# Kernel optimization log

Hardware: AMD Instinct MI355X
Metric: run time of the kernel (lower is better)

Reference implementation:

```python
import jax, jax.numpy as jnp
import numpy as np

K_MASK = -2.3819763e+38

B, T, D = 2, 2048, 2048
N_HEADS, N_KV, HEAD_DIM = 16, 8, 128
SCALAR = 0.08838834764831845  # head_dim ** -0.5
ROPE_BASE = 10000


def rms_norm(x, scale):
    # fp32 mean-of-squares, rsqrt, bf16 round-trip, then scale (as in QwemmaRMSNorm)
    x32 = x.astype(jnp.float32)
    var = jnp.mean(jnp.square(x32), axis=-1, keepdims=True)
    rescaled = (x32 * jax.lax.rsqrt(var + 1e-06)).astype(jnp.bfloat16)
    return rescaled * scale


def apply_rope(inputs, positions, base_frequency):
    head_dim = inputs.shape[-1]
    fraction = 2 * jnp.arange(0, head_dim // 2) / head_dim
    timescale = base_frequency ** fraction
    sinusoid = positions[..., jnp.newaxis] / timescale[jnp.newaxis, jnp.newaxis, :]
    sinusoid = sinusoid[..., jnp.newaxis, :]  # [B,T,1,H/2]
    sin = jnp.sin(sinusoid).astype(inputs.dtype)
    cos = jnp.cos(sinusoid).astype(inputs.dtype)
    first, second = jnp.split(inputs, 2, axis=-1)
    out = jnp.concatenate([first * cos - second * sin,
                           second * cos + first * sin], axis=-1)
    return out.astype(inputs.dtype)


def setup_inputs() -> dict:
    key = jax.random.key(0)
    ks = jax.random.split(key, 7)
    x = jax.random.normal(ks[0], (B, T, D), dtype=jnp.float32)
    segment_pos = jnp.broadcast_to(jnp.arange(T, dtype=jnp.int32)[None, :], (B, T))
    attn_mask = jnp.broadcast_to(jnp.tril(jnp.ones((T, T), dtype=bool))[None], (B, T, T))
    q_w = jax.random.normal(ks[1], (N_HEADS, D, HEAD_DIM), dtype=jnp.float32) * 0.02
    kv_w = jax.random.normal(ks[2], (2, N_KV, D, HEAD_DIM), dtype=jnp.float32) * 0.02
    o_w = jax.random.normal(ks[3], (N_HEADS, HEAD_DIM, D), dtype=jnp.float32) * 0.02
    q_scale = 1.0 + 0.1 * jax.random.normal(ks[4], (HEAD_DIM,), dtype=jnp.float32)
    k_scale = 1.0 + 0.1 * jax.random.normal(ks[5], (HEAD_DIM,), dtype=jnp.float32)
    return {"x": x, "segment_pos": segment_pos, "attn_mask": attn_mask,
            "q_w": q_w, "kv_w": kv_w, "o_w": o_w,
            "q_scale": q_scale, "k_scale": k_scale}


def reference(x, segment_pos, attn_mask, q_w, kv_w, o_w, q_scale, k_scale):
    # projections
    q = jnp.einsum('BTD,NDH->BTNH', x, q_w)
    k, v = jnp.einsum('BSD,CKDH->CBSKH', x, kv_w)
    # QK RMSNorm + RoPE
    q = apply_rope(rms_norm(q, q_scale), segment_pos, ROPE_BASE)
    k = apply_rope(rms_norm(k, k_scale), segment_pos, ROPE_BASE)
    # GQA: [B,T,N,H] -> [B,T,K,G,H]
    b, t, n, h = q.shape
    g = n // N_KV
    q = q.reshape((b, t, N_KV, g, h))
    logits = jnp.einsum('BTKGH,BSKH->BTKGS', q, k)
    logits = (logits.astype(jnp.float32) * SCALAR).astype(jnp.bfloat16)
    s = logits.shape[-1]
    logits = logits.reshape((b, t, n, s))
    padded = jnp.where(jnp.expand_dims(attn_mask, -2), logits, K_MASK)
    probs = jax.nn.softmax(padded.astype(jnp.float32), axis=-1).astype(k.dtype)
    probs = probs.reshape((b, t, N_KV, g, s))
    encoded = jnp.einsum('BTKGS,BSKH->BTKGH', probs, v)
    encoded = encoded.reshape((b, t, n, h))
    return jnp.einsum('BTNH,NHD->BTD', encoded, o_w)


if __name__ == '__main__':
    out = reference(**setup_inputs())
    print(out.shape, out.dtype)
```

## Files before the change

### kernel.cpp

```cpp
#include <hip/hip_runtime.h>

typedef unsigned short u16;
typedef __attribute__((ext_vector_type(4))) float f32x4;
typedef __attribute__((ext_vector_type(8))) short s16x8;

#define SCALAR_F 0.08838834764831845f
#define KMASKF (-1e30f)

__device__ __forceinline__ u16 f2b(float f){
  unsigned u = __float_as_uint(f);
  unsigned r = u + 0x7FFFu + ((u>>16)&1u);
  return (u16)(r>>16);
}
__device__ __forceinline__ float b2f(u16 h){ return __uint_as_float(((unsigned)h)<<16); }

__device__ __forceinline__ f32x4 mfma16(s16x8 a, s16x8 b, f32x4 c){
  return __builtin_amdgcn_mfma_f32_16x16x32_bf16(a, b, c, 0, 0, 0);
}

__device__ __forceinline__ void glds16(const u16* g, u16* l){
  __builtin_amdgcn_global_load_lds((const __attribute__((address_space(1))) unsigned*)g,
                                   (__attribute__((address_space(3))) unsigned*)l, 16, 0, 0);
}

__global__ __launch_bounds__(256) void cvt_f32_bf16(const float* __restrict__ in, u16* __restrict__ out){
  int i = blockIdx.x*256 + threadIdx.x;
  const float4* p = (const float4*)in;
  float4 a = p[2*i], b = p[2*i+1];
  s16x8 r;
  r[0]=(short)f2b(a.x); r[1]=(short)f2b(a.y); r[2]=(short)f2b(a.z); r[3]=(short)f2b(a.w);
  r[4]=(short)f2b(b.x); r[5]=(short)f2b(b.y); r[6]=(short)f2b(b.z); r[7]=(short)f2b(b.w);
  *(s16x8*)(out + (size_t)i*8) = r;
}

__global__ __launch_bounds__(256) void build_wqkvt(const float* __restrict__ qw, const float* __restrict__ kvw,
                                                   u16* __restrict__ out){
  __shared__ float t[64][65];
  int head = blockIdx.z;
  int d0 = blockIdx.y*64, h0 = blockIdx.x*64;
  const float* src; int colbase;
  if (head < 16){ src = qw + (size_t)head*2048*128; colbase = head*128; }
  else if (head < 24){ int k = head-16; src = kvw + (size_t)k*2048*128; colbase = 2048 + k*128; }
  else { int k = head-24; src = kvw + (size_t)(8+k)*2048*128; colbase = 3072 + k*128; }
  int tid = threadIdx.x;
  #pragma unroll
  for (int p=0;p<16;p++){ int e = p*256+tid; int r = e>>6, c = e&63;
    t[r][c] = src[(size_t)(d0+r)*128 + h0 + c]; }
  __syncthreads();
  #pragma unroll
  for (int p=0;p<16;p++){ int e = p*256+tid; int c = e>>6, r = e&63;
    out[(size_t)(colbase + h0 + c)*2048 + d0 + r] = f2b(t[r][c]); }
}

__global__ __launch_bounds__(256) void tr2048(const float* __restrict__ src, u16* __restrict__ out){
  __shared__ float t[64][65];
  int r0 = blockIdx.y*64, c0 = blockIdx.x*64;
  int tid = threadIdx.x;
  #pragma unroll
  for (int p=0;p<16;p++){ int e = p*256+tid; int r = e>>6, c = e&63;
    t[r][c] = src[(size_t)(r0+r)*2048 + c0 + c]; }
  __syncthreads();
  #pragma unroll
  for (int p=0;p<16;p++){ int e = p*256+tid; int c = e>>6, r = e&63;
    out[(size_t)(c0+c)*2048 + r0 + r] = f2b(t[r][c]); }
}

__global__ __launch_bounds__(256) void rope_table(float* __restrict__ table){
  int tid = blockIdx.x*256 + threadIdx.x;
  int pos = tid>>6, i = tid&63;
  float ts = powf(10000.f, (float)i * (1.f/64.f));
  float ang = (float)pos / ts;
  ((float2*)table)[tid] = make_float2(sinf(ang), cosf(ang));
}

template<bool OUTBF16>
__global__ __launch_bounds__(256) void gemm_bt(const u16* __restrict__ A, const u16* __restrict__ Bt,
                                               void* __restrict__ C, int K, int ldc){
  __shared__ u16 As[128*64];
  __shared__ u16 Bs[128*64];
  const int tid = threadIdx.x, w = tid>>6, l = tid&63;
  const int wm = w>>1, wn = w&1;
  const int l15 = l&15, lg = l>>4, l7 = l&7;
  const size_t m0 = (size_t)blockIdx.y*128, n0 = (size_t)blockIdx.x*128;
  const f32x4 z4 = {0.f,0.f,0.f,0.f};
  f32x4 acc[4][4];
  #pragma unroll
  for (int m=0;m<4;m++)
    #pragma unroll
    for (int n=0;n<4;n++) acc[m][n] = z4;
  const char* AsB = (const char*)As; const char* BsB = (const char*)Bs;
  int colsw[2];
  colsw[0] = (lg*16) ^ (l7<<4);
  colsw[1] = (64 + lg*16) ^ (l7<<4);
  int arow[4], brow[4];
  #pragma unroll
  for (int m=0;m<4;m++){ arow[m] = (wm*64 + m*16 + l15)*128; brow[m] = (wn*64 + m*16 + l15)*128; }
  const int sgl = l7 ^ (l>>3);
  for (int k0=0;k0<K;k0+=64){
    #pragma unroll
    for (int i=0;i<4;i++){
      int slot = (w*4+i)*64 + l;
      int row = slot>>3;
      glds16(A  + (m0+row)*K + k0 + sgl*8, (u16*)As + slot*8);
      glds16(Bt + (n0+row)*K + k0 + sgl*8, (u16*)Bs + slot*8);
    }
    __syncthreads();
    #pragma unroll
    for (int kb=0;kb<2;kb++){
      s16x8 af[4], bf[4];
      #pragma unroll
      for (int m=0;m<4;m++) af[m] = *(const s16x8*)(AsB + arow[m] + colsw[kb]);
      #pragma unroll
      for (int n=0;n<4;n++) bf[n] = *(const s16x8*)(BsB + brow[n] + colsw[kb]);
      #pragma unroll
      for (int m=0;m<4;m++)
        #pragma unroll
        for (int n=0;n<4;n++)
          acc[m][n] = mfma16(af[m], bf[n], acc[m][n]);
    }
    __syncthreads();
  }
  #pragma unroll
  for (int m=0;m<4;m++)
    #pragma unroll
    for (int n=0;n<4;n++)
      #pragma unroll
      for (int r=0;r<4;r++){
        size_t row = m0 + wm*64 + m*16 + lg*4 + r;
        size_t col = n0 + wn*64 + n*16 + l15;
        if (OUTBF16) ((u16*)C)[row*ldc + col] = f2b(acc[m][n][r]);
        else ((float*)C)[row*ldc + col] = acc[m][n][r];
      }
}

__global__ __launch_bounds__(256) void norm_rope(const u16* __restrict__ qkv, const float* __restrict__ table,
                                                 const float* __restrict__ scale, const int* __restrict__ segpos,
                                                 u16* __restrict__ dst, int nhl2, int colbase, float mult){
  int w = threadIdx.x>>6, l = threadIdx.x&63;
  int rid = blockIdx.x*4 + w;
  int bt = rid >> nhl2;
  int n  = rid & ((1<<nhl2)-1);
  int b = bt >> 11, t = bt & 2047;
  const u16* src = qkv + (size_t)bt*4096 + colbase + n*128;
  float x1 = b2f(src[l]), x2 = b2f(src[64+l]);
  float ss = x1*x1 + x2*x2;
  #pragma unroll
  for (int off=32; off; off>>=1) ss += __shfl_xor(ss, off);
  float rs = rsqrtf(ss*(1.f/128.f) + 1e-6f);
  float v1 = x1*rs*scale[l], v2 = x2*rs*scale[64+l];
  int pos = segpos[bt];
  float2 sc = ((const float2*)table)[pos*64 + l];
  float o1 = (v1*sc.y - v2*sc.x)*mult;
  float o2 = (v2*sc.y + v1*sc.x)*mult;
  u16* d = dst + (((size_t)((b<<nhl2) + n))*2048 + t)*128;
  d[l] = f2b(o1); d[64+l] = f2b(o2);
}

__global__ __launch_bounds__(256) void vtr(const u16* __restrict__ qkv, u16* __restrict__ vt){
  __shared__ float t[64][65];
  int bk = blockIdx.z;
  int t0 = blockIdx.y*64, d0 = blockIdx.x*64;
  int b = bk>>3, kv = bk&7;
  int tid = threadIdx.x;
  #pragma unroll
  for (int p=0;p<16;p++){ int e = p*256+tid; int r = e>>6, c = e&63;
    t[r][c] = b2f(qkv[(size_t)(b*2048 + t0 + r)*4096 + 3072 + kv*128 + d0 + c]); }
  __syncthreads();
  #pragma unroll
  for (int p=0;p<16;p++){ int e = p*256+tid; int c = e>>6, r = e&63;
    vt[((size_t)bk*128 + d0 + c)*2048 + t0 + r] = f2b(t[r][c]); }
}

__global__ __launch_bounds__(256,4) void attn_kern(const u16* __restrict__ qn, const u16* __restrict__ kn,
                                                   const u16* __restrict__ vt, u16* __restrict__ enc){
  __shared__ u16 Ks[64*128];
  __shared__ u16 Vs[128*64];
  __shared__ u16 Ps[4*16*64];
  const int idx = blockIdx.x;
  const int qb = 31 - (idx>>5);
  const int hb = idx & 31;
  const int hn = hb & 15, b = hb >> 4;
  const int t0 = qb*64;
  const int kv = hn>>1;
  const int tid = threadIdx.x, w = tid>>6, l = tid&63;
  const int l15 = l&15, lg = l>>4;
  const u16* qh = qn + ((size_t)(b*16+hn))*2048*128;
  const u16* kh = kn + ((size_t)(b*8+kv))*2048*128;
  const u16* vh = vt + ((size_t)(b*8+kv))*128*2048;
  const int qr0 = t0 + w*16;

  s16x8 qf[4];
  #pragma unroll
  for (int kb=0;kb<4;kb++)
    qf[kb] = *(const s16x8*)(qh + (size_t)(qr0 + l15)*128 + kb*32 + lg*8);

  const f32x4 z4 = {0.f,0.f,0.f,0.f};
  f32x4 o[8];
  #pragma unroll
  for (int dn=0;dn<8;dn++) o[dn] = z4;
  float mrow[4], lp[4];
  #pragma unroll
  for (int r=0;r<4;r++){ mrow[r] = KMASKF; lp[r] = 0.f; }

  const char* KsB = (const char*)Ks;
  const char* VsB = (const char*)Vs;
  char* PsB = (char*)Ps + w*2048;

  const int ntiles = qb + 1;
  for (int it=0; it<ntiles; ++it){
    int s0 = it*64;
    #pragma unroll
    for (int i=0;i<4;i++){
      int slot = (w*4+i)*64 + l;
      { int row = slot>>4, g = slot&15, gl = g ^ (row&7);
        glds16(kh + (size_t)(s0+row)*128 + gl*8, Ks + slot*8); }
      { int row = slot>>3, g = slot&7, gl = g ^ (row&7);
        glds16(vh + (size_t)row*2048 + s0 + gl*8, Vs + slot*8); }
    }
    __syncthreads();

    f32x4 sa[4];
    #pragma unroll
    for (int nc=0;nc<4;nc++) sa[nc] = z4;
    #pragma unroll
    for (int kb=0;kb<4;kb++){
      s16x8 kf[4];
      #pragma unroll
      for (int nc=0;nc<4;nc++){
        int srow = nc*16 + l15;
        int cb = (kb*64 + lg*16) ^ ((srow&7)<<4);
        kf[nc] = *(const s16x8*)(KsB + srow*256 + cb);
      }
      #pragma unroll
      for (int nc=0;nc<4;nc++)
        sa[nc] = mfma16(qf[kb], kf[nc], sa[nc]);
    }
    if (it == ntiles-1){
      #pragma unroll
      for (int nc=0;nc<4;nc++)
        #pragma unroll
        for (int r=0;r<4;r++){
          int row = qr0 + lg*4 + r;
          int col = s0 + nc*16 + l15;
          if (col > row) sa[nc][r] = KMASKF;
        }
    }
    #pragma unroll
    for (int r=0;r<4;r++){
      float pm = fmaxf(fmaxf(sa[0][r], sa[1][r]), fmaxf(sa[2][r], sa[3][r]));
      pm = fmaxf(pm, __shfl_xor(pm,1));
      pm = fmaxf(pm, __shfl_xor(pm,2));
      pm = fmaxf(pm, __shfl_xor(pm,4));
      pm = fmaxf(pm, __shfl_xor(pm,8));
      float mo = mrow[r];
      float mn = fmaxf(mo, pm);
      float sc = __expf(mo - mn);
      mrow[r] = mn;
      int rowp = lg*4 + r;
      float ls = 0.f;
      #pragma unroll
      for (int nc=0;nc<4;nc++){
        float p = __expf(sa[nc][r] - mn);
        ls += p;
        int cb = ((nc*16 + l15)*2) ^ ((rowp&7)<<4);
        *(u16*)(PsB + rowp*128 + cb) = f2b(p);
      }
      lp[r] = lp[r]*sc + ls;
      #pragma unroll
      for (int dn=0;dn<8;dn++) o[dn][r] *= sc;
    }
    asm volatile("" ::: "memory");
    #pragma unroll
    for (int kb=0;kb<2;kb++){
      int rowp = l15;
      int cbp = (kb*64 + lg*16) ^ ((rowp&7)<<4);
      s16x8 pf = *(const s16x8*)(PsB + rowp*128 + cbp);
      #pragma unroll
      for (int dn=0;dn<8;dn++){
        int vrow = dn*16 + l15;
        int cb = (kb*64 + lg*16) ^ ((vrow&7)<<4);
        s16x8 vf = *(const s16x8*)(VsB + vrow*128 + cb);
        o[dn] = mfma16(pf, vf, o[dn]);
      }
    }
    __syncthreads();
  }
  #pragma unroll
  for (int r=0;r<4;r++){
    float s = lp[r];
    s += __shfl_xor(s,1); s += __shfl_xor(s,2); s += __shfl_xor(s,4); s += __shfl_xor(s,8);
    lp[r] = 1.f/s;
  }
  #pragma unroll
  for (int dn=0;dn<8;dn++)
    #pragma unroll
    for (int r=0;r<4;r++){
      size_t row = (size_t)b*2048 + qr0 + lg*4 + r;
      size_t col = hn*128 + dn*16 + l15;
      enc[row*2048 + col] = f2b(o[dn][r]*lp[r]);
    }
}

extern "C" void kernel_launch(void* const* d_in, const int* in_sizes, int n_in,
                              void* d_out, int out_size, void* d_ws, size_t ws_size,
                              hipStream_t stream){
  const float* x      = (const float*)d_in[0];
  const int*   segpos = (const int*)d_in[1];
  const float* qw     = (const float*)d_in[3];
  const float* kvw    = (const float*)d_in[4];
  const float* ow     = (const float*)d_in[5];
  const float* qs     = (const float*)d_in[6];
  const float* ks     = (const float*)d_in[7];
  float* out = (float*)d_out;

  char* ws = (char*)d_ws;
  size_t off = 0;
  auto alloc = [&](size_t bytes)->void*{ void* p = ws + off; off += (bytes + 255) & ~(size_t)255; return p; };
  u16*   xb    = (u16*)alloc((size_t)4096*2048*2);
  u16*   wqkvt = (u16*)alloc((size_t)4096*2048*2);
  u16*   wot   = (u16*)alloc((size_t)2048*2048*2);
  u16*   qkv   = (u16*)alloc((size_t)4096*4096*2);
  u16*   qn    = (u16*)alloc((size_t)2*16*2048*128*2);
  u16*   kn    = (u16*)alloc((size_t)2*8*2048*128*2);
  u16*   vt    = (u16*)alloc((size_t)2*8*128*2048*2);
  u16*   enc   = (u16*)alloc((size_t)4096*2048*2);
  float* table = (float*)alloc((size_t)2048*64*2*4);

  cvt_f32_bf16<<<4096,256,0,stream>>>(x, xb);
  build_wqkvt<<<dim3(2,32,32),256,0,stream>>>(qw, kvw, wqkvt);
  tr2048<<<dim3(32,32),256,0,stream>>>(ow, wot);
  rope_table<<<512,256,0,stream>>>(table);
  gemm_bt<true><<<dim3(32,32),256,0,stream>>>(xb, wqkvt, qkv, 2048, 4096);
  norm_rope<<<16384,256,0,stream>>>(qkv, table, qs, segpos, qn, 4, 0,    SCALAR_F);
  norm_rope<<<8192, 256,0,stream>>>(qkv, table, ks, segpos, kn, 3, 2048, 1.0f);
  vtr<<<dim3(2,32,16),256,0,stream>>>(qkv, vt);
  attn_kern<<<1024,256,0,stream>>>(qn, kn, vt, enc);
  gemm_bt<false><<<dim3(16,32),256,0,stream>>>(enc, wot, out, 2048, 2048);
}
```

Measured before the change: 438.0 us.

## Pair causal query blocks per workgroup and double-buffer K/V tiles in LDS

Each attention workgroup now handles two query blocks, pp and 31-pp, so every workgroup runs exactly 33 KV tiles and the causal triangle's work is balanced. K/V tiles are double-buffered in LDS, and the next tile's global-to-LDS loads are issued before computing on the current one, overlapping memory with MFMA work. The grid is halved to 512 workgroups and launch bounds drop to 2 blocks per CU. The larger LDS footprint and fewer workgroups may reduce occupancy.

Result: faster. 384.7 us (-12.2%).

```diff
diff --git a/kernel.cpp b/kernel.cpp
--- a/kernel.cpp
+++ b/kernel.cpp
@@ -171,24 +171,24 @@
     vt[((size_t)bk*128 + d0 + c)*2048 + t0 + r] = f2b(t[r][c]); }
 }
 
-__global__ __launch_bounds__(256,4) void attn_kern(const u16* __restrict__ qn, const u16* __restrict__ kn,
+__global__ __launch_bounds__(256,2) void attn_kern(const u16* __restrict__ qn, const u16* __restrict__ kn,
                                                    const u16* __restrict__ vt, u16* __restrict__ enc){
-  __shared__ u16 Ks[64*128];
-  __shared__ u16 Vs[128*64];
+  __shared__ u16 Ks[2][64*128];
+  __shared__ u16 Vs[2][64*128];
   __shared__ u16 Ps[4*16*64];
   const int idx = blockIdx.x;
-  const int qb = 31 - (idx>>5);
+  const int pp = idx>>5;
   const int hb = idx & 31;
   const int hn = hb & 15, b = hb >> 4;
-  const int t0 = qb*64;
   const int kv = hn>>1;
   const int tid = threadIdx.x, w = tid>>6, l = tid&63;
   const int l15 = l&15, lg = l>>4;
   const u16* qh = qn + ((size_t)(b*16+hn))*2048*128;
   const u16* kh = kn + ((size_t)(b*8+kv))*2048*128;
   const u16* vh = vt + ((size_t)(b*8+kv))*128*2048;
-  const int qr0 = t0 + w*16;
-
+  const int qbA = pp, qbB = 31-pp;
+
+  int qr0 = qbA*64 + w*16;
   s16x8 qf[4];
   #pragma unroll
   for (int kb=0;kb<4;kb++)
@@ -202,22 +202,50 @@
   #pragma unroll
   for (int r=0;r<4;r++){ mrow[r] = KMASKF; lp[r] = 0.f; }
 
-  const char* KsB = (const char*)Ks;
-  const char* VsB = (const char*)Vs;
+  const char* KsB0 = (const char*)&Ks[0][0];
+  const char* VsB0 = (const char*)&Vs[0][0];
   char* PsB = (char*)Ps + w*2048;
 
-  const int ntiles = qb + 1;
-  for (int it=0; it<ntiles; ++it){
-    int s0 = it*64;
+  auto stage = [&](int s0, int bi){
     #pragma unroll
     for (int i=0;i<4;i++){
       int slot = (w*4+i)*64 + l;
       { int row = slot>>4, g = slot&15, gl = g ^ (row&7);
-        glds16(kh + (size_t)(s0+row)*128 + gl*8, Ks + slot*8); }
+        glds16(kh + (size_t)(s0+row)*128 + gl*8, &Ks[bi][0] + slot*8); }
       { int row = slot>>3, g = slot&7, gl = g ^ (row&7);
-        glds16(vh + (size_t)row*2048 + s0 + gl*8, Vs + slot*8); }
-    }
-    __syncthreads();
+        glds16(vh + (size_t)row*2048 + s0 + gl*8, &Vs[bi][0] + slot*8); }
+    }
+  };
+
+  auto epilogue = [&](int qr){
+    #pragma unroll
+    for (int r=0;r<4;r++){
+      float s = lp[r];
+      s += __shfl_xor(s,1); s += __shfl_xor(s,2); s += __shfl_xor(s,4); s += __shfl_xor(s,8);
+      lp[r] = 1.f/s;
+    }
+    #pragma unroll
+    for (int dn=0;dn<8;dn++)
+      #pragma unroll
+      for (int r=0;r<4;r++){
+        size_t row = (size_t)b*2048 + qr + lg*4 + r;
+        size_t col = hn*128 + dn*16 + l15;
+        enc[row*2048 + col] = f2b(o[dn][r]*lp[r]);
+      }
+  };
+
+  stage(0, 0);
+  __syncthreads();
+
+  int cur = 0;
+  for (int it=0; it<=32; ++it){
+    if (it < 32){
+      int s0n = (it+1 <= pp) ? (it+1)*64 : (it-pp)*64;
+      stage(s0n, cur^1);
+    }
+    const int s0 = (it <= pp) ? it*64 : (it-pp-1)*64;
+    const char* KsB = KsB0 + cur*16384;
+    const char* VsB = VsB0 + cur*16384;
 
     f32x4 sa[4];
     #pragma unroll
@@ -235,7 +263,7 @@
       for (int nc=0;nc<4;nc++)
         sa[nc] = mfma16(qf[kb], kf[nc], sa[nc]);
     }
-    if (it == ntiles-1){
+    if (it == pp || it == 32){
       #pragma unroll
       for (int nc=0;nc<4;nc++)
         #pragma unroll
@@ -283,22 +311,21 @@
         o[dn] = mfma16(pf, vf, o[dn]);
       }
     }
+    if (it == pp){
+      epilogue(qr0);
+      qr0 = qbB*64 + w*16;
+      #pragma unroll
+      for (int kb=0;kb<4;kb++)
+        qf[kb] = *(const s16x8*)(qh + (size_t)(qr0 + l15)*128 + kb*32 + lg*8);
+      #pragma unroll
+      for (int dn=0;dn<8;dn++) o[dn] = z4;
+      #pragma unroll
+      for (int r=0;r<4;r++){ mrow[r] = KMASKF; lp[r] = 0.f; }
+    }
     __syncthreads();
+    cur ^= 1;
   }
-  #pragma unroll
-  for (int r=0;r<4;r++){
-    float s = lp[r];
-    s += __shfl_xor(s,1); s += __shfl_xor(s,2); s += __shfl_xor(s,4); s += __shfl_xor(s,8);
-    lp[r] = 1.f/s;
-  }
-  #pragma unroll
-  for (int dn=0;dn<8;dn++)
-    #pragma unroll
-    for (int r=0;r<4;r++){
-      size_t row = (size_t)b*2048 + qr0 + lg*4 + r;
-      size_t col = hn*128 + dn*16 + l15;
-      enc[row*2048 + col] = f2b(o[dn][r]*lp[r]);
-    }
+  epilogue(qr0);
 }
 
 extern "C" void kernel_launch(void* const* d_in, const int* in_sizes, int n_in,
@@ -334,6 +361,6 @@
   norm_rope<<<16384,256,0,stream>>>(qkv, table, qs, segpos, qn, 4, 0,    SCALAR_F);
   norm_rope<<<8192, 256,0,stream>>>(qkv, table, ks, segpos, kn, 3, 2048, 1.0f);
   vtr<<<dim3(2,32,16),256,0,stream>>>(qkv, vt);
-  attn_kern<<<1024,256,0,stream>>>(qn, kn, vt, enc);
+  attn_kern<<<512,256,0,stream>>>(qn, kn, vt, enc);
   gemm_bt<false><<<dim3(16,32),256,0,stream>>>(enc, wot, out, 2048, 2048);
 }
```
